# Optimization experiments

Measured on AMD Instinct MI355X. Metric: run time of the kernel, lower is better.

Reference implementation:

```python
import jax, jax.numpy as jnp
from jax import lax
import numpy as np

K_IN, K_OUT, K_STATE = 64, 64, 256
T_PRE, T_FWD, BATCH = 64, 80, 4096


def setup_inputs() -> dict:
    key = jax.random.key(0)
    ks = jax.random.split(key, 13)
    s = 0.05  # param scale for numerical stability of the recurrences
    return {
        "pre_x": jax.random.normal(ks[0], (T_PRE, BATCH, K_IN), jnp.float32),
        "pre_y": jax.random.normal(ks[1], (T_PRE, BATCH, K_OUT), jnp.float32),
        "forward_x": jax.random.normal(ks[2], (T_FWD, BATCH, K_IN), jnp.float32),
        "A_w": jax.random.normal(ks[3], (K_STATE, K_STATE), jnp.float32) * s,
        "A_b": jax.random.normal(ks[4], (K_STATE,), jnp.float32) * s,
        "B_w": jax.random.normal(ks[5], (K_STATE, K_IN), jnp.float32) * s,
        "B_b": jax.random.normal(ks[6], (K_STATE,), jnp.float32) * s,
        "C_w": jax.random.normal(ks[7], (K_OUT, K_STATE), jnp.float32) * s,
        "C_b": jax.random.normal(ks[8], (K_OUT,), jnp.float32) * s,
        "W_ih": jax.random.normal(ks[9], (K_STATE, K_IN + K_OUT), jnp.float32) * s,
        "b_ih": jax.random.normal(ks[10], (K_STATE,), jnp.float32) * s,
        "W_hh": jax.random.normal(ks[11], (K_STATE, K_STATE), jnp.float32) * s,
        "b_hh": jax.random.normal(ks[12], (K_STATE,), jnp.float32) * s,
    }


def reference(pre_x, pre_y, forward_x, A_w, A_b, B_w, B_b, C_w, C_b,
              W_ih, b_ih, W_hh, b_hh):
    # --- encoder: single-layer tanh RNN over concat(pre_x, pre_y), h0 = 0 ---
    xy = jnp.concatenate([pre_x, pre_y], axis=2)          # [T_pre, B, k_in+k_out]
    # precompute input projection for all steps (one big GEMM)
    inp_proj = xy @ W_ih.T + b_ih                          # [T_pre, B, k_state]

    def rnn_step(h, u):
        h = jnp.tanh(u + h @ W_hh.T + b_hh)
        return h, None

    h0 = jnp.zeros((pre_x.shape[1], W_hh.shape[0]), pre_x.dtype)
    hn, _ = lax.scan(rnn_step, h0, inp_proj)               # hn: [B, k_state]

    # --- state-space rollout: h_t = A h_{t-1} + B x_t ; y_t = C h_t ---
    Bx = forward_x @ B_w.T + (A_b + B_b)                   # fold both biases once

    def ss_step(h, bx):
        h = h @ A_w.T + bx
        return h, h

    _, hs = lax.scan(ss_step, hn, Bx)                      # [T_fwd, B, k_state]
    return hs @ C_w.T + C_b                                # [T_fwd, B, k_out]
```

## Files before the change

kernel.cpp:

```cpp
#include <hip/hip_runtime.h>
#include <hip/hip_bf16.h>

typedef __attribute__((ext_vector_type(8))) short short8;
typedef __attribute__((ext_vector_type(4))) float f32x4;

#define T_PRE 64
#define T_FWD 80
#define BATCHN 4096

#define HP 264
#define IP 136

#define U_WRNN 0
#define U_WSS  98304
#define U_C    180224
#define U_END  196608
#define PREP_N 197120

__device__ __forceinline__ unsigned short bf1(float a) {
  unsigned ua = __float_as_uint(a);
  return (unsigned short)((ua + 0x7fffu + ((ua >> 16) & 1u)) >> 16);
}
__device__ __forceinline__ unsigned pk(float a, float b) {
  __hip_bfloat162 h = __float22bfloat162_rn(make_float2(a, b));
  unsigned u;
  __builtin_memcpy(&u, &h, 4);
  return u;
}
__device__ __forceinline__ float tanh_fast(float x) {
  float e = __expf(2.0f * x);
  return 1.0f - 2.0f * __builtin_amdgcn_rcpf(e + 1.0f);
}

__global__ void prep_kernel(const float* __restrict__ A_w, const float* __restrict__ A_b,
                            const float* __restrict__ B_w, const float* __restrict__ B_b,
                            const float* __restrict__ C_w,
                            const float* __restrict__ W_ih, const float* __restrict__ b_ih,
                            const float* __restrict__ W_hh, const float* __restrict__ b_hh,
                            unsigned short* __restrict__ ws) {
  int i = blockIdx.x * 256 + threadIdx.x;
  if (i < U_WSS) {
    int j = i / 384, k = i - j * 384;
    float v = (k < 256) ? W_hh[j * 256 + k] : W_ih[j * 128 + (k - 256)];
    ws[i] = bf1(v);
  } else if (i < U_C) {
    int ii = i - U_WSS;
    int j = ii / 320, k = ii - j * 320;
    float v = (k < 256) ? A_w[j * 256 + k] : B_w[j * 64 + (k - 256)];
    ws[i] = bf1(v);
  } else if (i < U_END) {
    int ii = i - U_C;
    int o = ii >> 8, k = ii & 255;
    ws[i] = bf1(C_w[o * 256 + k]);
  } else if (i < PREP_N) {
    float* fb = (float*)(ws + U_END);
    int j = i - U_END;
    fb[j] = (j < 256) ? (b_ih[j] + b_hh[j]) : (A_b[j - 256] + B_b[j - 256]);
  }
}

__global__ __launch_bounds__(512, 1) void rnn_ss_kernel(
    const float* __restrict__ pre_x, const float* __restrict__ pre_y,
    const float* __restrict__ fwd_x, const float* __restrict__ C_b,
    const unsigned short* __restrict__ ws, float* __restrict__ out) {
  __shared__ unsigned short hbuf[2][16 * HP];
  __shared__ unsigned short ibuf[2][16 * IP];

  const int tid = threadIdx.x;
  const int lane = tid & 63;
  const int w = tid >> 6;
  const int col = lane & 15;
  const int q = lane >> 4;
  const int r0 = blockIdx.x * 16;
  const int srow = (tid & 255) >> 4;
  const int sc4 = tid & 15;
  const bool xhalf = (tid >= 256);

#pragma unroll
  for (int it = 0; it < 2; ++it) {
    int i = tid + it * 512;
    int r = i >> 6, c = (i & 63) * 4;
    *(uint2*)&hbuf[0][r * HP + c] = make_uint2(0u, 0u);
  }

  const float* fbias = (const float*)(ws + U_END);
  int cur = 0;

  {
    short8 wf[2][12];
#pragma unroll
    for (int mt = 0; mt < 2; ++mt)
#pragma unroll
      for (int kf = 0; kf < 12; ++kf)
        wf[mt][kf] = *(const short8*)(ws + U_WRNN +
                       (size_t)(w * 32 + mt * 16 + col) * 384 + kf * 32 + q * 8);
    f32x4 br[2];
#pragma unroll
    for (int mt = 0; mt < 2; ++mt)
      br[mt] = *(const f32x4*)(fbias + w * 32 + mt * 16 + q * 4);

    {
      f32x4 v = xhalf ? *(const f32x4*)(pre_x + (size_t)(r0 + srow) * 64 + sc4 * 4)
                      : *(const f32x4*)(pre_y + (size_t)(r0 + srow) * 64 + sc4 * 4);
      *(uint2*)&ibuf[0][srow * IP + (xhalf ? 0 : 64) + sc4 * 4] =
          make_uint2(pk(v[0], v[1]), pk(v[2], v[3]));
    }

    for (int t = 0; t < T_PRE; ++t) {
      f32x4 nv;
      bool do_stage = true;
      if (t < T_PRE - 1) {
        nv = xhalf ? *(const f32x4*)(pre_x + ((size_t)(t + 1) * BATCHN + r0 + srow) * 64 + sc4 * 4)
                   : *(const f32x4*)(pre_y + ((size_t)(t + 1) * BATCHN + r0 + srow) * 64 + sc4 * 4);
      } else if (xhalf) {
        nv = *(const f32x4*)(fwd_x + (size_t)(r0 + srow) * 64 + sc4 * 4);
      } else {
        do_stage = false;
      }
      __syncthreads();
      const unsigned short* hc = hbuf[cur];
      const unsigned short* ic = ibuf[cur];
      short8 bfr[12];
#pragma unroll
      for (int kf = 0; kf < 8; ++kf)
        bfr[kf] = *(const short8*)&hc[col * HP + kf * 32 + q * 8];
#pragma unroll
      for (int kf = 8; kf < 12; ++kf)
        bfr[kf] = *(const short8*)&ic[col * IP + (kf - 8) * 32 + q * 8];
      f32x4 acc[2];
#pragma unroll
      for (int mt = 0; mt < 2; ++mt) acc[mt] = br[mt];
#pragma unroll
      for (int kf = 0; kf < 12; ++kf)
#pragma unroll
        for (int mt = 0; mt < 2; ++mt)
          acc[mt] = __builtin_amdgcn_mfma_f32_16x16x32_bf16(wf[mt][kf], bfr[kf], acc[mt], 0, 0, 0);
      unsigned short* hn_ = hbuf[cur ^ 1];
#pragma unroll
      for (int mt = 0; mt < 2; ++mt) {
        float t0 = tanh_fast(acc[mt][0]), t1 = tanh_fast(acc[mt][1]);
        float t2 = tanh_fast(acc[mt][2]), t3 = tanh_fast(acc[mt][3]);
        *(uint2*)&hn_[col * HP + w * 32 + mt * 16 + q * 4] =
            make_uint2(pk(t0, t1), pk(t2, t3));
      }
      if (do_stage)
        *(uint2*)&ibuf[cur ^ 1][srow * IP + (xhalf ? 0 : 64) + sc4 * 4] =
            make_uint2(pk(nv[0], nv[1]), pk(nv[2], nv[3]));
      cur ^= 1;
    }
  }

  {
    short8 sf[2][10];
#pragma unroll
    for (int mt = 0; mt < 2; ++mt)
#pragma unroll
      for (int kf = 0; kf < 10; ++kf)
        sf[mt][kf] = *(const short8*)(ws + U_WSS +
                       (size_t)(w * 32 + mt * 16 + col) * 320 + kf * 32 + q * 8);
    f32x4 bs[2];
#pragma unroll
    for (int mt = 0; mt < 2; ++mt)
      bs[mt] = *(const f32x4*)(fbias + 256 + w * 32 + mt * 16 + q * 4);
    short8 cf[8];
    f32x4 cb;
    if (w < 4) {
#pragma unroll
      for (int kf = 0; kf < 8; ++kf)
        cf[kf] = *(const short8*)(ws + U_C + (size_t)(w * 16 + col) * 256 + kf * 32 + q * 8);
      cb = *(const f32x4*)(C_b + w * 16 + q * 4);
    }

    for (int i = 0; i < T_FWD; ++i) {
      f32x4 nv;
      if (i < T_FWD - 1 && xhalf)
        nv = *(const f32x4*)(fwd_x + ((size_t)(i + 1) * BATCHN + r0 + srow) * 64 + sc4 * 4);
      __syncthreads();
      const unsigned short* hc = hbuf[cur];
      const unsigned short* ic = ibuf[cur];
      short8 bfr[10];
#pragma unroll
      for (int kf = 0; kf < 8; ++kf)
        bfr[kf] = *(const short8*)&hc[col * HP + kf * 32 + q * 8];
#pragma unroll
      for (int kf = 8; kf < 10; ++kf)
        bfr[kf] = *(const short8*)&ic[col * IP + (kf - 8) * 32 + q * 8];
      f32x4 acc[2];
#pragma unroll
      for (int mt = 0; mt < 2; ++mt) acc[mt] = bs[mt];
#pragma unroll
      for (int kf = 0; kf < 10; ++kf)
#pragma unroll
        for (int mt = 0; mt < 2; ++mt)
          acc[mt] = __builtin_amdgcn_mfma_f32_16x16x32_bf16(sf[mt][kf], bfr[kf], acc[mt], 0, 0, 0);
      if (w < 4 && i >= 1) {
        f32x4 y = cb;
#pragma unroll
        for (int kf = 0; kf < 8; ++kf)
          y = __builtin_amdgcn_mfma_f32_16x16x32_bf16(cf[kf], bfr[kf], y, 0, 0, 0);
        *(f32x4*)(out + ((size_t)(i - 1) * BATCHN + r0 + col) * 64 + w * 16 + q * 4) = y;
      }
      unsigned short* hn_ = hbuf[cur ^ 1];
#pragma unroll
      for (int mt = 0; mt < 2; ++mt)
        *(uint2*)&hn_[col * HP + w * 32 + mt * 16 + q * 4] =
            make_uint2(pk(acc[mt][0], acc[mt][1]), pk(acc[mt][2], acc[mt][3]));
      if (i < T_FWD - 1 && xhalf)
        *(uint2*)&ibuf[cur ^ 1][srow * IP + sc4 * 4] =
            make_uint2(pk(nv[0], nv[1]), pk(nv[2], nv[3]));
      cur ^= 1;
    }

    __syncthreads();
    if (w < 4) {
      const unsigned short* hc = hbuf[cur];
      short8 bfr[8];
#pragma unroll
      for (int kf = 0; kf < 8; ++kf)
        bfr[kf] = *(const short8*)&hc[col * HP + kf * 32 + q * 8];
      f32x4 y = cb;
#pragma unroll
      for (int kf = 0; kf < 8; ++kf)
        y = __builtin_amdgcn_mfma_f32_16x16x32_bf16(cf[kf], bfr[kf], y, 0, 0, 0);
      *(f32x4*)(out + ((size_t)(T_FWD - 1) * BATCHN + r0 + col) * 64 + w * 16 + q * 4) = y;
    }
  }
}

extern "C" void kernel_launch(void* const* d_in, const int* in_sizes, int n_in,
                              void* d_out, int out_size, void* d_ws, size_t ws_size,
                              hipStream_t stream) {
  const float* pre_x = (const float*)d_in[0];
  const float* pre_y = (const float*)d_in[1];
  const float* fwd_x = (const float*)d_in[2];
  const float* A_w   = (const float*)d_in[3];
  const float* A_b   = (const float*)d_in[4];
  const float* B_w   = (const float*)d_in[5];
  const float* B_b   = (const float*)d_in[6];
  const float* C_w   = (const float*)d_in[7];
  const float* C_b   = (const float*)d_in[8];
  const float* W_ih  = (const float*)d_in[9];
  const float* b_ih  = (const float*)d_in[10];
  const float* W_hh  = (const float*)d_in[11];
  const float* b_hh  = (const float*)d_in[12];
  unsigned short* ws = (unsigned short*)d_ws;
  float* out = (float*)d_out;

  prep_kernel<<<(PREP_N + 255) / 256, 256, 0, stream>>>(
      A_w, A_b, B_w, B_b, C_w, W_ih, b_ih, W_hh, b_hh, ws);
  rnn_ss_kernel<<<BATCHN / 16, 512, 0, stream>>>(pre_x, pre_y, fwd_x, C_b, ws, out);
}
```

Baseline: 295.3 us.

## Halve block to 256 threads with each wave computing 64 state rows

The recurrence kernel now uses 4 waves per block instead of 8. Each wave holds twice as many weight fragments in registers and computes 64 output rows per step, and each thread stages both the x and y input tiles. This cuts barrier participants and makes every wave share the output projection, at the cost of higher register pressure. It also leaves only one wave per SIMD, so MFMA latency can no longer be hidden by a second wave.

```diff
diff --git a/kernel.cpp b/kernel.cpp
--- a/kernel.cpp
+++ b/kernel.cpp
@@ -59,7 +59,7 @@
   }
 }
 
-__global__ __launch_bounds__(512, 1) void rnn_ss_kernel(
+__global__ __launch_bounds__(256, 1) void rnn_ss_kernel(
     const float* __restrict__ pre_x, const float* __restrict__ pre_y,
     const float* __restrict__ fwd_x, const float* __restrict__ C_b,
     const unsigned short* __restrict__ ws, float* __restrict__ out) {
@@ -72,13 +72,12 @@
   const int col = lane & 15;
   const int q = lane >> 4;
   const int r0 = blockIdx.x * 16;
-  const int srow = (tid & 255) >> 4;
+  const int srow = tid >> 4;
   const int sc4 = tid & 15;
-  const bool xhalf = (tid >= 256);
-
-#pragma unroll
-  for (int it = 0; it < 2; ++it) {
-    int i = tid + it * 512;
+
+#pragma unroll
+  for (int it = 0; it < 4; ++it) {
+    int i = tid + it * 256;
     int r = i >> 6, c = (i & 63) * 4;
     *(uint2*)&hbuf[0][r * HP + c] = make_uint2(0u, 0u);
   }
@@ -87,35 +86,35 @@
   int cur = 0;
 
   {
-    short8 wf[2][12];
-#pragma unroll
-    for (int mt = 0; mt < 2; ++mt)
+    short8 wf[4][12];
+#pragma unroll
+    for (int mt = 0; mt < 4; ++mt)
 #pragma unroll
       for (int kf = 0; kf < 12; ++kf)
         wf[mt][kf] = *(const short8*)(ws + U_WRNN +
-                       (size_t)(w * 32 + mt * 16 + col) * 384 + kf * 32 + q * 8);
-    f32x4 br[2];
-#pragma unroll
-    for (int mt = 0; mt < 2; ++mt)
-      br[mt] = *(const f32x4*)(fbias + w * 32 + mt * 16 + q * 4);
+                       (size_t)(w * 64 + mt * 16 + col) * 384 + kf * 32 + q * 8);
+    f32x4 br[4];
+#pragma unroll
+    for (int mt = 0; mt < 4; ++mt)
+      br[mt] = *(const f32x4*)(fbias + w * 64 + mt * 16 + q * 4);
 
     {
-      f32x4 v = xhalf ? *(const f32x4*)(pre_x + (size_t)(r0 + srow) * 64 + sc4 * 4)
-                      : *(const f32x4*)(pre_y + (size_t)(r0 + srow) * 64 + sc4 * 4);
-      *(uint2*)&ibuf[0][srow * IP + (xhalf ? 0 : 64) + sc4 * 4] =
-          make_uint2(pk(v[0], v[1]), pk(v[2], v[3]));
+      f32x4 vx = *(const f32x4*)(pre_x + (size_t)(r0 + srow) * 64 + sc4 * 4);
+      f32x4 vy = *(const f32x4*)(pre_y + (size_t)(r0 + srow) * 64 + sc4 * 4);
+      *(uint2*)&ibuf[0][srow * IP + sc4 * 4] =
+          make_uint2(pk(vx[0], vx[1]), pk(vx[2], vx[3]));
+      *(uint2*)&ibuf[0][srow * IP + 64 + sc4 * 4] =
+          make_uint2(pk(vy[0], vy[1]), pk(vy[2], vy[3]));
     }
 
     for (int t = 0; t < T_PRE; ++t) {
-      f32x4 nv;
-      bool do_stage = true;
-      if (t < T_PRE - 1) {
-        nv = xhalf ? *(const f32x4*)(pre_x + ((size_t)(t + 1) * BATCHN + r0 + srow) * 64 + sc4 * 4)
-                   : *(const f32x4*)(pre_y + ((size_t)(t + 1) * BATCHN + r0 + srow) * 64 + sc4 * 4);
-      } else if (xhalf) {
-        nv = *(const f32x4*)(fwd_x + (size_t)(r0 + srow) * 64 + sc4 * 4);
+      f32x4 nvx, nvy;
+      const bool sy = (t < T_PRE - 1);
+      if (sy) {
+        nvx = *(const f32x4*)(pre_x + ((size_t)(t + 1) * BATCHN + r0 + srow) * 64 + sc4 * 4);
+        nvy = *(const f32x4*)(pre_y + ((size_t)(t + 1) * BATCHN + r0 + srow) * 64 + sc4 * 4);
       } else {
-        do_stage = false;
+        nvx = *(const f32x4*)(fwd_x + (size_t)(r0 + srow) * 64 + sc4 * 4);
       }
       __syncthreads();
       const unsigned short* hc = hbuf[cur];
@@ -127,53 +126,52 @@
 #pragma unroll
       for (int kf = 8; kf < 12; ++kf)
         bfr[kf] = *(const short8*)&ic[col * IP + (kf - 8) * 32 + q * 8];
-      f32x4 acc[2];
-#pragma unroll
-      for (int mt = 0; mt < 2; ++mt) acc[mt] = br[mt];
+      f32x4 acc[4];
+#pragma unroll
+      for (int mt = 0; mt < 4; ++mt) acc[mt] = br[mt];
 #pragma unroll
       for (int kf = 0; kf < 12; ++kf)
 #pragma unroll
-        for (int mt = 0; mt < 2; ++mt)
+        for (int mt = 0; mt < 4; ++mt)
           acc[mt] = __builtin_amdgcn_mfma_f32_16x16x32_bf16(wf[mt][kf], bfr[kf], acc[mt], 0, 0, 0);
       unsigned short* hn_ = hbuf[cur ^ 1];
 #pragma unroll
-      for (int mt = 0; mt < 2; ++mt) {
+      for (int mt = 0; mt < 4; ++mt) {
         float t0 = tanh_fast(acc[mt][0]), t1 = tanh_fast(acc[mt][1]);
         float t2 = tanh_fast(acc[mt][2]), t3 = tanh_fast(acc[mt][3]);
-        *(uint2*)&hn_[col * HP + w * 32 + mt * 16 + q * 4] =
+        *(uint2*)&hn_[col * HP + w * 64 + mt * 16 + q * 4] =
             make_uint2(pk(t0, t1), pk(t2, t3));
       }
-      if (do_stage)
-        *(uint2*)&ibuf[cur ^ 1][srow * IP + (xhalf ? 0 : 64) + sc4 * 4] =
-            make_uint2(pk(nv[0], nv[1]), pk(nv[2], nv[3]));
+      *(uint2*)&ibuf[cur ^ 1][srow * IP + sc4 * 4] =
+          make_uint2(pk(nvx[0], nvx[1]), pk(nvx[2], nvx[3]));
+      if (sy)
+        *(uint2*)&ibuf[cur ^ 1][srow * IP + 64 + sc4 * 4] =
+            make_uint2(pk(nvy[0], nvy[1]), pk(nvy[2], nvy[3]));
       cur ^= 1;
     }
   }
 
   {
-    short8 sf[2][10];
-#pragma unroll
-    for (int mt = 0; mt < 2; ++mt)
+    short8 sf[4][10];
+#pragma unroll
+    for (int mt = 0; mt < 4; ++mt)
 #pragma unroll
       for (int kf = 0; kf < 10; ++kf)
         sf[mt][kf] = *(const short8*)(ws + U_WSS +
-                       (size_t)(w * 32 + mt * 16 + col) * 320 + kf * 32 + q * 8);
-    f32x4 bs[2];
-#pragma unroll
-    for (int mt = 0; mt < 2; ++mt)
-      bs[mt] = *(const f32x4*)(fbias + 256 + w * 32 + mt * 16 + q * 4);
+                       (size_t)(w * 64 + mt * 16 + col) * 320 + kf * 32 + q * 8);
+    f32x4 bs[4];
+#pragma unroll
+    for (int mt = 0; mt < 4; ++mt)
+      bs[mt] = *(const f32x4*)(fbias + 256 + w * 64 + mt * 16 + q * 4);
     short8 cf[8];
-    f32x4 cb;
-    if (w < 4) {
-#pragma unroll
-      for (int kf = 0; kf < 8; ++kf)
-        cf[kf] = *(const short8*)(ws + U_C + (size_t)(w * 16 + col) * 256 + kf * 32 + q * 8);
-      cb = *(const f32x4*)(C_b + w * 16 + q * 4);
-    }
+#pragma unroll
+    for (int kf = 0; kf < 8; ++kf)
+      cf[kf] = *(const short8*)(ws + U_C + (size_t)(w * 16 + col) * 256 + kf * 32 + q * 8);
+    f32x4 cb = *(const f32x4*)(C_b + w * 16 + q * 4);
 
     for (int i = 0; i < T_FWD; ++i) {
       f32x4 nv;
-      if (i < T_FWD - 1 && xhalf)
+      if (i < T_FWD - 1)
         nv = *(const f32x4*)(fwd_x + ((size_t)(i + 1) * BATCHN + r0 + srow) * 64 + sc4 * 4);
       __syncthreads();
       const unsigned short* hc = hbuf[cur];
@@ -185,15 +183,15 @@
 #pragma unroll
       for (int kf = 8; kf < 10; ++kf)
         bfr[kf] = *(const short8*)&ic[col * IP + (kf - 8) * 32 + q * 8];
-      f32x4 acc[2];
-#pragma unroll
-      for (int mt = 0; mt < 2; ++mt) acc[mt] = bs[mt];
+      f32x4 acc[4];
+#pragma unroll
+      for (int mt = 0; mt < 4; ++mt) acc[mt] = bs[mt];
 #pragma unroll
       for (int kf = 0; kf < 10; ++kf)
 #pragma unroll
-        for (int mt = 0; mt < 2; ++mt)
+        for (int mt = 0; mt < 4; ++mt)
           acc[mt] = __builtin_amdgcn_mfma_f32_16x16x32_bf16(sf[mt][kf], bfr[kf], acc[mt], 0, 0, 0);
-      if (w < 4 && i >= 1) {
+      if (i >= 1) {
         f32x4 y = cb;
 #pragma unroll
         for (int kf = 0; kf < 8; ++kf)
@@ -202,17 +200,17 @@
       }
       unsigned short* hn_ = hbuf[cur ^ 1];
 #pragma unroll
-      for (int mt = 0; mt < 2; ++mt)
-        *(uint2*)&hn_[col * HP + w * 32 + mt * 16 + q * 4] =
+      for (int mt = 0; mt < 4; ++mt)
+        *(uint2*)&hn_[col * HP + w * 64 + mt * 16 + q * 4] =
             make_uint2(pk(acc[mt][0], acc[mt][1]), pk(acc[mt][2], acc[mt][3]));
-      if (i < T_FWD - 1 && xhalf)
+      if (i < T_FWD - 1)
         *(uint2*)&ibuf[cur ^ 1][srow * IP + sc4 * 4] =
             make_uint2(pk(nv[0], nv[1]), pk(nv[2], nv[3]));
       cur ^= 1;
     }
 
     __syncthreads();
-    if (w < 4) {
+    {
       const unsigned short* hc = hbuf[cur];
       short8 bfr[8];
 #pragma unroll
@@ -248,5 +246,5 @@
 
   prep_kernel<<<(PREP_N + 255) / 256, 256, 0, stream>>>(
       A_w, A_b, B_w, B_b, C_w, W_ih, b_ih, W_hh, b_hh, ws);
-  rnn_ss_kernel<<<BATCHN / 16, 512, 0, stream>>>(pre_x, pre_y, fwd_x, C_b, ws, out);
-}
+  rnn_ss_kernel<<<BATCHN / 16, 256, 0, stream>>>(pre_x, pre_y, fwd_x, C_b, ws, out);
+}
```

Measured after the change: 334.8 us. +13.4%, slower.
